# Kernel tuning notes

Hardware: AMD Instinct MI355X
Metric: run time of the kernel (lower is better)

## Reference

```python
import math
import jax, jax.numpy as jnp
import numpy as np

NUM_HEADS = 16
D_MODEL = 1024
B, S = 1, 4096


def setup_inputs() -> dict:
    key = jax.random.key(0)
    ks = jax.random.split(key, 10)
    sc = 1.0 / math.sqrt(D_MODEL)
    # causal mask: 1.0 where masked (strictly upper triangular), 0.0 elsewhere
    causal = jnp.triu(jnp.ones((S, S), dtype=jnp.float32), k=1)
    return {
        "query": jax.random.normal(ks[0], (B, S, D_MODEL), dtype=jnp.float32),
        "mask": jnp.broadcast_to(causal, (B, S, S)),
        "Wq": jax.random.normal(ks[1], (D_MODEL, D_MODEL), dtype=jnp.float32) * sc,
        "bq": jax.random.normal(ks[2], (D_MODEL,), dtype=jnp.float32) * sc,
        "Wk": jax.random.normal(ks[3], (D_MODEL, D_MODEL), dtype=jnp.float32) * sc,
        "bk": jax.random.normal(ks[4], (D_MODEL,), dtype=jnp.float32) * sc,
        "Wv": jax.random.normal(ks[5], (D_MODEL, D_MODEL), dtype=jnp.float32) * sc,
        "bv": jax.random.normal(ks[6], (D_MODEL,), dtype=jnp.float32) * sc,
        "Wo": jax.random.normal(ks[7], (D_MODEL, D_MODEL), dtype=jnp.float32) * sc,
        "bo": jax.random.normal(ks[8], (D_MODEL,), dtype=jnp.float32) * sc,
    }


def _split_heads(x, H, dh):
    # [B,S,D] -> [B,H,S,dh]; head h owns channels [h*dh:(h+1)*dh] (matches the
    # module's transpose->reshape->transpose trick, which equals the contiguous split)
    b, s, _ = x.shape
    return x.reshape(b, s, H, dh).transpose(0, 2, 1, 3)


def reference(query, mask, Wq, bq, Wk, bk, Wv, bv, Wo, bo):
    H = NUM_HEADS
    B_, S_, D = query.shape
    dh = D // H
    q = _split_heads(query @ Wq.T + bq, H, dh)   # [B,H,S,dh]
    k = _split_heads(query @ Wk.T + bk, H, dh)   # self-attention: key = query
    v = _split_heads(query @ Wv.T + bv, H, dh)
    # materialized scores [B,H,S,S]
    scores = jnp.einsum("bhqd,bhkd->bhqk", q, k)
    # mask applied BEFORE the 1/sqrt(d_head) scaling, faithful to the source
    scores = scores + mask[:, None, :, :] * (-1e9)
    attn = jax.nn.softmax(scores / math.sqrt(dh), axis=-1)  # [B,H,S,S]
    out = jnp.einsum("bhqk,bhkd->bhqd", attn, v)            # [B,H,S,dh]
    combined = out.transpose(0, 2, 1, 3).reshape(B_, S_, D)  # [B,S,D]
    return combined @ Wo.T + bo
```

## Files before the change

### kernel.cpp

```cpp
#include <hip/hip_runtime.h>

typedef __bf16 bf16x8 __attribute__((ext_vector_type(8)));
typedef __bf16 bf16x4 __attribute__((ext_vector_type(4)));
typedef float f32x4 __attribute__((ext_vector_type(4)));

typedef const __attribute__((address_space(1))) void* as1_cvp;
typedef __attribute__((address_space(3))) void* as3_vp;
__device__ __forceinline__ void g2l16(const void* g, void* l) {
  __builtin_amdgcn_global_load_lds((as1_cvp)(uintptr_t)g, (as3_vp)(uintptr_t)l, 16, 0, 0);
}

__global__ __launch_bounds__(256) void cast_f32_to_bf16(const float* __restrict__ in,
                                                        __bf16* __restrict__ out, int n4) {
  for (int idx = blockIdx.x * 256 + threadIdx.x; idx < n4; idx += gridDim.x * 256) {
    float4 f = reinterpret_cast<const float4*>(in)[idx];
    bf16x4 t;
    t.x = (__bf16)f.x; t.y = (__bf16)f.y; t.z = (__bf16)f.z; t.w = (__bf16)f.w;
    reinterpret_cast<bf16x4*>(out)[idx] = t;
  }
}

__global__ __launch_bounds__(256) void cast3_f32_to_bf16(const float* __restrict__ w0,
                                                         const float* __restrict__ w1,
                                                         const float* __restrict__ w2,
                                                         __bf16* __restrict__ out, int n4,
                                                         float qs) {
  const float* src = blockIdx.y == 0 ? w0 : (blockIdx.y == 1 ? w1 : w2);
  const float s = blockIdx.y == 0 ? qs : 1.0f;
  __bf16* dst = out + (size_t)blockIdx.y * (size_t)n4 * 4;
  for (int idx = blockIdx.x * 256 + threadIdx.x; idx < n4; idx += gridDim.x * 256) {
    float4 f = reinterpret_cast<const float4*>(src)[idx];
    bf16x4 t;
    t.x = (__bf16)(f.x * s); t.y = (__bf16)(f.y * s);
    t.z = (__bf16)(f.z * s); t.w = (__bf16)(f.w * s);
    reinterpret_cast<bf16x4*>(dst)[idx] = t;
  }
}

template <int BM, typename OUT_T, bool VT_FUSE>
__global__ __launch_bounds__(256) void gemm_bt(const __bf16* __restrict__ A,
                                               const __bf16* __restrict__ B,
                                               const float* __restrict__ b0,
                                               const float* __restrict__ b1,
                                               const float* __restrict__ b2,
                                               OUT_T* __restrict__ C,
                                               __bf16* __restrict__ Vt,
                                               int K, int ldc, float qs) {
  constexpr int MT = BM / 32;
  __shared__ __align__(16) __bf16 Alds[BM][64];
  __shared__ __align__(16) __bf16 Blds[128][64];
  const int tid = threadIdx.x;
  const int wave = tid >> 6, lane = tid & 63;
  const int wm = wave & 1, wn = wave >> 1;
  const int mlane = lane & 15, quad = lane >> 4;
  const int m0 = blockIdx.x * BM, n0 = blockIdx.y * 128;

  f32x4 acc[MT][4] = {};
  constexpr int AN = BM * 8 / 256;

  for (int k0 = 0; k0 < K; k0 += 64) {
#pragma unroll
    for (int j = 0; j < AN; j++) {
      int c = j * 256 + tid;
      g2l16(&A[(size_t)(m0 + (c >> 3)) * K + k0 + (c & 7) * 8], &Alds[0][0] + c * 8);
    }
#pragma unroll
    for (int j = 0; j < 4; j++) {
      int c = j * 256 + tid;
      g2l16(&B[(size_t)(n0 + (c >> 3)) * K + k0 + (c & 7) * 8], &Blds[0][0] + c * 8);
    }
    __syncthreads();
    bf16x8 af[MT][2], bfr[4][2];
#pragma unroll
    for (int mt = 0; mt < MT; mt++)
#pragma unroll
      for (int s = 0; s < 2; s++)
        af[mt][s] = *reinterpret_cast<const bf16x8*>(
            &Alds[wm * (BM / 2) + mt * 16 + mlane][s * 32 + quad * 8]);
#pragma unroll
    for (int nt = 0; nt < 4; nt++)
#pragma unroll
      for (int s = 0; s < 2; s++)
        bfr[nt][s] = *reinterpret_cast<const bf16x8*>(
            &Blds[wn * 64 + nt * 16 + mlane][s * 32 + quad * 8]);
#pragma unroll
    for (int mt = 0; mt < MT; mt++)
#pragma unroll
      for (int nt = 0; nt < 4; nt++)
#pragma unroll
        for (int s = 0; s < 2; s++)
          acc[mt][nt] = __builtin_amdgcn_mfma_f32_16x16x32_bf16(af[mt][s], bfr[nt][s],
                                                                acc[mt][nt], 0, 0, 0);
    __syncthreads();
  }

  const int region = n0 >> 10;
  const float* bp = region == 0 ? b0 : (region == 1 ? b1 : b2);
  const float bs = (region == 0) ? qs : 1.0f;
  float bvs[4];
#pragma unroll
  for (int nt = 0; nt < 4; nt++)
    bvs[nt] = bp[(n0 + wn * 64 + nt * 16 + mlane) & 1023] * bs;

  if (VT_FUSE && region == 2) {
#pragma unroll
    for (int mt = 0; mt < MT; mt++)
#pragma unroll
      for (int nt = 0; nt < 4; nt++) {
        int vcol = ((n0 + wn * 64 + nt * 16 + mlane) & 1023);
        int row0 = m0 + wm * (BM / 2) + mt * 16 + quad * 4;
        bf16x4 t;
#pragma unroll
        for (int r = 0; r < 4; r++) t[r] = (__bf16)(acc[mt][nt][r] + bvs[nt]);
        *reinterpret_cast<bf16x4*>(&Vt[(size_t)vcol * 4096 + row0]) = t;
      }
  } else {
#pragma unroll
    for (int mt = 0; mt < MT; mt++)
#pragma unroll
      for (int nt = 0; nt < 4; nt++) {
        int col = n0 + wn * 64 + nt * 16 + mlane;
#pragma unroll
        for (int r = 0; r < 4; r++) {
          int row = m0 + wm * (BM / 2) + mt * 16 + quad * 4 + r;
          C[(size_t)row * ldc + col] = (OUT_T)(acc[mt][nt][r] + bvs[nt]);
        }
      }
  }
}

__global__ __launch_bounds__(512, 4) void flash_attn(const __bf16* __restrict__ QK,
                                                     const __bf16* __restrict__ Vt,
                                                     __bf16* __restrict__ O, int S) {
  const int LDQ = 2048, D = 1024;
  __shared__ __align__(16) __bf16 Klds[128][72];
  __shared__ __align__(16) __bf16 Vlds[64][136];
  __shared__ __align__(16) __bf16 Plds[8][16][72];
  const int tid = threadIdx.x;
  const int wave = tid >> 6, lane = tid & 63;
  const int mlane = lane & 15, quad = lane >> 4;
  const int half = wave >> 2, rw = wave & 3;
  const int b = blockIdx.x, h = blockIdx.y;

  for (int pass = 0; pass < 2; ++pass) {
    const int qb = pass ? b : (63 - b);
    const int qbase = qb * 64 + rw * 16;

    bf16x8 qf[2];
#pragma unroll
    for (int s = 0; s < 2; s++)
      qf[s] = *reinterpret_cast<const bf16x8*>(
          &QK[(size_t)(qbase + mlane) * LDQ + h * 64 + s * 32 + quad * 8]);

    f32x4 o[4] = {};
    float lrow[4] = {0.f, 0.f, 0.f, 0.f};

    const int nkb = qb / 2 + 1;
    for (int kb = 0; kb < nkb; ++kb) {
#pragma unroll
      for (int j = 0; j < 2; j++) {
        int c = j * 512 + tid, r = c >> 3, cc = c & 7;
        *reinterpret_cast<uint4*>(&Klds[r][cc * 8]) = *reinterpret_cast<const uint4*>(
            &QK[(size_t)(kb * 128 + r) * LDQ + 1024 + h * 64 + cc * 8]);
      }
#pragma unroll
      for (int j = 0; j < 2; j++) {
        int c = j * 512 + tid, r = c >> 4, cc = c & 15;
        *reinterpret_cast<uint4*>(&Vlds[r][cc * 8]) = *reinterpret_cast<const uint4*>(
            &Vt[(size_t)(h * 64 + r) * S + kb * 128 + cc * 8]);
      }
      __syncthreads();

      f32x4 sc[4];
#pragma unroll
      for (int nt = 0; nt < 4; nt++) {
        f32x4 a = {};
#pragma unroll
        for (int s = 0; s < 2; s++) {
          bf16x8 bk = *reinterpret_cast<const bf16x8*>(
              &Klds[half * 64 + nt * 16 + mlane][s * 32 + quad * 8]);
          a = __builtin_amdgcn_mfma_f32_16x16x32_bf16(qf[s], bk, a, 0, 0, 0);
        }
        sc[nt] = a;
      }

      const bool maskTile = (kb == nkb - 1);
#pragma unroll
      for (int r = 0; r < 4; r++) {
        if (maskTile) {
          const int qg = qbase + quad * 4 + r;
#pragma unroll
          for (int nt = 0; nt < 4; nt++) {
            int kg = kb * 128 + half * 64 + nt * 16 + mlane;
            if (kg > qg) sc[nt][r] = -INFINITY;
          }
        }
        float ls = 0.f;
#pragma unroll
        for (int nt = 0; nt < 4; nt++) {
          float p = __builtin_amdgcn_exp2f(sc[nt][r]);
          sc[nt][r] = p;
          ls += p;
        }
        lrow[r] += ls;
#pragma unroll
        for (int nt = 0; nt < 4; nt++)
          Plds[wave][quad * 4 + r][nt * 16 + mlane] = (__bf16)sc[nt][r];
      }

#pragma unroll
      for (int s = 0; s < 2; s++) {
        bf16x8 pf =
            *reinterpret_cast<const bf16x8*>(&Plds[wave][mlane][s * 32 + quad * 8]);
#pragma unroll
        for (int nt = 0; nt < 4; nt++) {
          bf16x8 vf = *reinterpret_cast<const bf16x8*>(
              &Vlds[nt * 16 + mlane][half * 64 + s * 32 + quad * 8]);
          o[nt] = __builtin_amdgcn_mfma_f32_16x16x32_bf16(pf, vf, o[nt], 0, 0, 0);
        }
      }
      __syncthreads();
    }

    float* osc = (float*)&Klds[0][0];
    float* lsc = (float*)&Vlds[0][0];
    if (half == 1) {
      const int ob = (rw * 64 + lane) * 18, lb = (rw * 64 + lane) * 5;
#pragma unroll
      for (int nt = 0; nt < 4; nt++)
#pragma unroll
        for (int r = 0; r < 4; r++) osc[ob + nt * 4 + r] = o[nt][r];
#pragma unroll
      for (int r = 0; r < 4; r++) lsc[lb + r] = lrow[r];
    }
    __syncthreads();
    if (half == 0) {
      const int ob = (rw * 64 + lane) * 18, lb = (rw * 64 + lane) * 5;
#pragma unroll
      for (int nt = 0; nt < 4; nt++)
#pragma unroll
        for (int r = 0; r < 4; r++) o[nt][r] += osc[ob + nt * 4 + r];
#pragma unroll
      for (int r = 0; r < 4; r++) {
        float l = lrow[r] + lsc[lb + r];
#pragma unroll
        for (int off = 1; off < 16; off <<= 1) l += __shfl_xor(l, off, 64);
        float inv = 1.0f / l;
        int row = qbase + quad * 4 + r;
#pragma unroll
        for (int nt = 0; nt < 4; nt++)
          O[(size_t)row * D + h * 64 + nt * 16 + mlane] = (__bf16)(o[nt][r] * inv);
      }
    }
    __syncthreads();
  }
}

extern "C" void kernel_launch(void* const* d_in, const int* in_sizes, int n_in,
                              void* d_out, int out_size, void* d_ws, size_t ws_size,
                              hipStream_t stream) {
  const float* query = (const float*)d_in[0];
  const float* Wq = (const float*)d_in[2];
  const float* bq = (const float*)d_in[3];
  const float* Wk = (const float*)d_in[4];
  const float* bk = (const float*)d_in[5];
  const float* Wv = (const float*)d_in[6];
  const float* bv = (const float*)d_in[7];
  const float* Wo = (const float*)d_in[8];
  const float* bo = (const float*)d_in[9];
  float* out = (float*)d_out;

  const int S = 4096, D = 1024;
  const float SCL = 0.125f * 1.44269504088896340736f;
  char* ws = (char*)d_ws;
  __bf16* Xb   = (__bf16*)(ws);
  __bf16* Cb   = (__bf16*)(ws);
  __bf16* Wqkv = (__bf16*)(ws + (8u << 20));
  __bf16* Wob  = (__bf16*)(ws + (14u << 20));
  __bf16* QKb  = (__bf16*)(ws + (16u << 20));
  __bf16* Vt   = (__bf16*)(ws + (32u << 20));

  cast_f32_to_bf16<<<1024, 256, 0, stream>>>(query, Xb, S * D / 4);
  cast3_f32_to_bf16<<<dim3(256, 3), 256, 0, stream>>>(Wq, Wk, Wv, Wqkv, D * D / 4, SCL);
  cast_f32_to_bf16<<<256, 256, 0, stream>>>(Wo, Wob, D * D / 4);

  gemm_bt<128, __bf16, true><<<dim3(S / 128, 3 * D / 128), 256, 0, stream>>>(
      Xb, Wqkv, bq, bk, bv, QKb, Vt, D, 2048, SCL);

  flash_attn<<<dim3(32, 16), 512, 0, stream>>>(QKb, Vt, Cb, S);

  gemm_bt<64, float, false><<<dim3(S / 64, D / 128), 256, 0, stream>>>(
      Cb, Wob, bo, bo, bo, out, nullptr, D, D, 1.0f);
}
```

Before: 281.7 us.

## Compute transposed scores so P stays in registers, dropping the LDS round-trip

Swaps the MFMA operands so the score tile comes out transposed, with each lane holding a key column for one query. The exponentiated probabilities can then feed the PV MFMA directly as bf16x4 register operands through the 16x16x16 instruction, which removes the Plds staging buffer and its LDS stores and loads. K tiles are now loaded straight into unpadded LDS with global_load_lds, and row sums and output stores become vectorized per lane. The risks are LDS bank conflicts on the unpadded K layout and twice as many smaller MFMA instructions for PV.

```diff
diff --git a/kernel.cpp b/kernel.cpp
--- a/kernel.cpp
+++ b/kernel.cpp
@@ -3,6 +3,7 @@
 typedef __bf16 bf16x8 __attribute__((ext_vector_type(8)));
 typedef __bf16 bf16x4 __attribute__((ext_vector_type(4)));
 typedef float f32x4 __attribute__((ext_vector_type(4)));
+typedef short s16x4 __attribute__((ext_vector_type(4)));
 
 typedef const __attribute__((address_space(1))) void* as1_cvp;
 typedef __attribute__((address_space(3))) void* as3_vp;
@@ -133,9 +134,11 @@
                                                      const __bf16* __restrict__ Vt,
                                                      __bf16* __restrict__ O, int S) {
   const int LDQ = 2048, D = 1024;
-  __shared__ __align__(16) __bf16 Klds[128][72];
-  __shared__ __align__(16) __bf16 Vlds[64][136];
-  __shared__ __align__(16) __bf16 Plds[8][16][72];
+  __shared__ __align__(16) char smem[33792];
+  __bf16(*Klds)[64] = reinterpret_cast<__bf16(*)[64]>(smem);
+  __bf16(*Vlds)[136] = reinterpret_cast<__bf16(*)[136]>(smem + 16384);
+  float* scr = reinterpret_cast<float*>(smem);
+
   const int tid = threadIdx.x;
   const int wave = tid >> 6, lane = tid & 63;
   const int mlane = lane & 15, quad = lane >> 4;
@@ -153,15 +156,15 @@
           &QK[(size_t)(qbase + mlane) * LDQ + h * 64 + s * 32 + quad * 8]);
 
     f32x4 o[4] = {};
-    float lrow[4] = {0.f, 0.f, 0.f, 0.f};
+    float lsum = 0.f;
 
     const int nkb = qb / 2 + 1;
     for (int kb = 0; kb < nkb; ++kb) {
 #pragma unroll
       for (int j = 0; j < 2; j++) {
-        int c = j * 512 + tid, r = c >> 3, cc = c & 7;
-        *reinterpret_cast<uint4*>(&Klds[r][cc * 8]) = *reinterpret_cast<const uint4*>(
-            &QK[(size_t)(kb * 128 + r) * LDQ + 1024 + h * 64 + cc * 8]);
+        int c = j * 512 + tid;
+        g2l16(&QK[(size_t)(kb * 128 + (c >> 3)) * LDQ + 1024 + h * 64 + (c & 7) * 8],
+              smem + c * 16);
       }
 #pragma unroll
       for (int j = 0; j < 2; j++) {
@@ -177,79 +180,71 @@
         f32x4 a = {};
 #pragma unroll
         for (int s = 0; s < 2; s++) {
-          bf16x8 bk = *reinterpret_cast<const bf16x8*>(
+          bf16x8 kf = *reinterpret_cast<const bf16x8*>(
               &Klds[half * 64 + nt * 16 + mlane][s * 32 + quad * 8]);
-          a = __builtin_amdgcn_mfma_f32_16x16x32_bf16(qf[s], bk, a, 0, 0, 0);
+          a = __builtin_amdgcn_mfma_f32_16x16x32_bf16(kf, qf[s], a, 0, 0, 0);
         }
         sc[nt] = a;
       }
 
       const bool maskTile = (kb == nkb - 1);
-#pragma unroll
-      for (int r = 0; r < 4; r++) {
-        if (maskTile) {
-          const int qg = qbase + quad * 4 + r;
-#pragma unroll
-          for (int nt = 0; nt < 4; nt++) {
-            int kg = kb * 128 + half * 64 + nt * 16 + mlane;
+      const int qg = qbase + mlane;
+      s16x4 pf[4];
+#pragma unroll
+      for (int nt = 0; nt < 4; nt++) {
+        bf16x4 pb;
+#pragma unroll
+        for (int r = 0; r < 4; r++) {
+          if (maskTile) {
+            int kg = kb * 128 + half * 64 + nt * 16 + quad * 4 + r;
             if (kg > qg) sc[nt][r] = -INFINITY;
           }
-        }
-        float ls = 0.f;
-#pragma unroll
-        for (int nt = 0; nt < 4; nt++) {
           float p = __builtin_amdgcn_exp2f(sc[nt][r]);
-          sc[nt][r] = p;
-          ls += p;
-        }
-        lrow[r] += ls;
-#pragma unroll
-        for (int nt = 0; nt < 4; nt++)
-          Plds[wave][quad * 4 + r][nt * 16 + mlane] = (__bf16)sc[nt][r];
-      }
-
-#pragma unroll
-      for (int s = 0; s < 2; s++) {
-        bf16x8 pf =
-            *reinterpret_cast<const bf16x8*>(&Plds[wave][mlane][s * 32 + quad * 8]);
-#pragma unroll
-        for (int nt = 0; nt < 4; nt++) {
-          bf16x8 vf = *reinterpret_cast<const bf16x8*>(
-              &Vlds[nt * 16 + mlane][half * 64 + s * 32 + quad * 8]);
-          o[nt] = __builtin_amdgcn_mfma_f32_16x16x32_bf16(pf, vf, o[nt], 0, 0, 0);
+          lsum += p;
+          pb[r] = (__bf16)p;
+        }
+        pf[nt] = *reinterpret_cast<s16x4*>(&pb);
+      }
+
+#pragma unroll
+      for (int nt = 0; nt < 4; nt++) {
+#pragma unroll
+        for (int mt = 0; mt < 4; mt++) {
+          bf16x4 vv = *reinterpret_cast<const bf16x4*>(
+              &Vlds[mt * 16 + mlane][half * 64 + nt * 16 + quad * 4]);
+          o[mt] = __builtin_amdgcn_mfma_f32_16x16x16bf16_1k(
+              *reinterpret_cast<s16x4*>(&vv), pf[nt], o[mt], 0, 0, 0);
         }
       }
       __syncthreads();
     }
 
-    float* osc = (float*)&Klds[0][0];
-    float* lsc = (float*)&Vlds[0][0];
+    const int sbase = (rw * 64 + lane) * 17;
     if (half == 1) {
-      const int ob = (rw * 64 + lane) * 18, lb = (rw * 64 + lane) * 5;
-#pragma unroll
-      for (int nt = 0; nt < 4; nt++)
-#pragma unroll
-        for (int r = 0; r < 4; r++) osc[ob + nt * 4 + r] = o[nt][r];
-#pragma unroll
-      for (int r = 0; r < 4; r++) lsc[lb + r] = lrow[r];
+#pragma unroll
+      for (int mt = 0; mt < 4; mt++)
+#pragma unroll
+        for (int r = 0; r < 4; r++) scr[sbase + mt * 4 + r] = o[mt][r];
+      scr[sbase + 16] = lsum;
     }
     __syncthreads();
     if (half == 0) {
-      const int ob = (rw * 64 + lane) * 18, lb = (rw * 64 + lane) * 5;
-#pragma unroll
-      for (int nt = 0; nt < 4; nt++)
-#pragma unroll
-        for (int r = 0; r < 4; r++) o[nt][r] += osc[ob + nt * 4 + r];
-#pragma unroll
-      for (int r = 0; r < 4; r++) {
-        float l = lrow[r] + lsc[lb + r];
-#pragma unroll
-        for (int off = 1; off < 16; off <<= 1) l += __shfl_xor(l, off, 64);
-        float inv = 1.0f / l;
-        int row = qbase + quad * 4 + r;
-#pragma unroll
-        for (int nt = 0; nt < 4; nt++)
-          O[(size_t)row * D + h * 64 + nt * 16 + mlane] = (__bf16)(o[nt][r] * inv);
+#pragma unroll
+      for (int mt = 0; mt < 4; mt++)
+#pragma unroll
+        for (int r = 0; r < 4; r++) o[mt][r] += scr[sbase + mt * 4 + r];
+      float l = lsum + scr[sbase + 16];
+      l += __shfl_xor(l, 16, 64);
+      l += __shfl_xor(l, 32, 64);
+      float inv = 1.0f / l;
+      const int row = qbase + mlane;
+#pragma unroll
+      for (int mt = 0; mt < 4; mt++) {
+        bf16x4 t;
+#pragma unroll
+        for (int r = 0; r < 4; r++) t[r] = (__bf16)(o[mt][r] * inv);
+        *reinterpret_cast<bf16x4*>(
+            &O[(size_t)row * D + h * 64 + mt * 16 + quad * 4]) = t;
       }
     }
     __syncthreads();
```

Result: no change. 286.7 us (+1.8%).
